# Optimization experiments

Hardware: AMD Instinct MI355X
Metric: run time of the kernel (lower is better)

Reference implementation:

```python
import jax, jax.numpy as jnp
import numpy as np

B, H, W, C = 64, 56, 56, 128
WIN, SHIFT, NH = 7, 3, 4
HD = C // NH
N = WIN * WIN
nWh, nWw = H // WIN, W // WIN
nW = nWh * nWw
MLP_H = 4 * C


def _rel_pos_index():
    # same construction as WindowAttention.__init__
    coords = np.stack(np.meshgrid(np.arange(WIN), np.arange(WIN), indexing='ij')).reshape(2, -1)
    rel = coords[:, :, None] - coords[:, None, :]
    rel = rel.transpose(1, 2, 0).copy()
    rel[..., 0] += WIN - 1
    rel[..., 1] += WIN - 1
    rel[..., 0] *= 2 * WIN - 1
    return rel.sum(-1)  # (N, N) int


def _attn_mask():
    # standard SW-MSA mask (0 / -100 like the torch reference)
    img = np.zeros((H, W))
    cnt = 0
    for hs in (slice(0, -WIN), slice(-WIN, -SHIFT), slice(-SHIFT, None)):
        for ws in (slice(0, -WIN), slice(-WIN, -SHIFT), slice(-SHIFT, None)):
            img[hs, ws] = cnt
            cnt += 1
    m = img.reshape(nWh, WIN, nWw, WIN).transpose(0, 2, 1, 3).reshape(nW, N)
    diff = m[:, None, :] - m[:, :, None]
    return np.where(diff != 0, -100.0, 0.0).astype(np.float32)  # (nW, N, N)


def _ln(x, g, b):
    mu = x.mean(-1, keepdims=True)
    var = ((x - mu) ** 2).mean(-1, keepdims=True)
    return (x - mu) / jnp.sqrt(var + 1e-5) * g + b


def setup_inputs() -> dict:
    key = jax.random.key(0)
    ks = jax.random.split(key, 6)
    s = 0.02
    return {
        'x': jax.random.normal(ks[0], (B, H * W, C), jnp.float32),
        'ln1_g': jnp.ones((C,), jnp.float32),
        'ln1_b': jnp.zeros((C,), jnp.float32),
        'qkv_w': jax.random.normal(ks[1], (3 * C, C), jnp.float32) * s,
        'qkv_b': jnp.zeros((3 * C,), jnp.float32),
        'rpb_table': jax.random.normal(ks[2], ((2 * WIN - 1) ** 2, NH), jnp.float32) * s,
        'proj_w': jax.random.normal(ks[3], (C, C), jnp.float32) * s,
        'proj_b': jnp.zeros((C,), jnp.float32),
        'ln2_g': jnp.ones((C,), jnp.float32),
        'ln2_b': jnp.zeros((C,), jnp.float32),
        'fc1_w': jax.random.normal(ks[4], (MLP_H, C), jnp.float32) * s,
        'fc1_b': jnp.zeros((MLP_H,), jnp.float32),
        'fc2_w': jax.random.normal(ks[5], (C, MLP_H), jnp.float32) * s,
        'fc2_b': jnp.zeros((C,), jnp.float32),
    }


def reference(x, ln1_g, ln1_b, qkv_w, qkv_b, rpb_table, proj_w, proj_b,
              ln2_g, ln2_b, fc1_w, fc1_b, fc2_w, fc2_b):
    rpi = jnp.asarray(_rel_pos_index())          # (N, N)
    mask = jnp.asarray(_attn_mask())             # (nW, N, N)

    shortcut = x
    h = _ln(x, ln1_g, ln1_b).reshape(B, H, W, C)
    # cyclic shift
    h = jnp.roll(h, (-SHIFT, -SHIFT), axis=(1, 2))
    # window partition -> (B*nW, N, C)
    wins = h.reshape(B, nWh, WIN, nWw, WIN, C).transpose(0, 1, 3, 2, 4, 5).reshape(B * nW, N, C)

    # window attention
    qkv = (wins @ qkv_w.T + qkv_b).reshape(B * nW, N, 3, NH, HD).transpose(2, 0, 3, 1, 4)
    q, k, v = qkv[0] * (HD ** -0.5), qkv[1], qkv[2]   # (B*nW, NH, N, HD)
    attn = jnp.einsum('bhnd,bhmd->bhnm', q, k)
    bias = rpb_table[rpi.reshape(-1)].reshape(N, N, NH).transpose(2, 0, 1)  # (NH, N, N)
    attn = attn + bias[None]
    attn = attn.reshape(B, nW, NH, N, N) + mask[None, :, None]
    attn = jax.nn.softmax(attn.reshape(B * nW, NH, N, N), axis=-1)
    o = jnp.einsum('bhnm,bhmd->bhnd', attn, v).transpose(0, 2, 1, 3).reshape(B * nW, N, C)
    o = o @ proj_w.T + proj_b

    # window reverse + reverse shift
    o = o.reshape(B, nWh, nWw, WIN, WIN, C).transpose(0, 1, 3, 2, 4, 5).reshape(B, H, W, C)
    o = jnp.roll(o, (SHIFT, SHIFT), axis=(1, 2)).reshape(B, H * W, C)

    x = shortcut + o
    # MLP residual (exact GELU, as nn.GELU default)
    h2 = _ln(x, ln2_g, ln2_b)
    h2 = jax.nn.gelu(h2 @ fc1_w.T + fc1_b, approximate=False) @ fc2_w.T + fc2_b
    return x + h2
```

## Files before the change

### kernel.cpp

```cpp
#include <hip/hip_runtime.h>
#include <math.h>

#define B_  64
#define Cc  128
#define L_  3136

typedef __bf16 b8v __attribute__((ext_vector_type(8)));
typedef __bf16 b4v __attribute__((ext_vector_type(4)));
typedef float  f4v __attribute__((ext_vector_type(4)));

__device__ __forceinline__ f4v mfma16(b8v a, b8v b, f4v c) {
    return __builtin_amdgcn_mfma_f32_16x16x32_bf16(a, b, c, 0, 0, 0);
}
__device__ __forceinline__ int region(int h, int w) {
    int a = (h < 49) ? 0 : ((h < 53) ? 1 : 2);
    int b = (w < 49) ? 0 : ((w < 53) ? 1 : 2);
    return a * 3 + b;
}

__global__ __launch_bounds__(256) void prep_kernel(
    const float* __restrict__ qkv_w, const float* __restrict__ proj_w,
    const float* __restrict__ fc1_w, const float* __restrict__ fc2_w,
    const float* __restrict__ rpb,
    __bf16* __restrict__ wsb, float* __restrict__ bm)
{
    int i = blockIdx.x * 256 + threadIdx.x;
    if      (i <  49152) wsb[i] = (__bf16)qkv_w[i];
    else if (i <  65536) wsb[i] = (__bf16)proj_w[i - 49152];
    else if (i < 131072) wsb[i] = (__bf16)fc1_w[i - 65536];
    else if (i < 196608) wsb[i] = (__bf16)fc2_w[i - 131072];
    else {
        int idx = i - 196608;
        int jj = idx & 63, ii = (idx >> 6) & 63, h = (idx >> 12) & 3, wt = idx >> 14;
        float v;
        if (jj >= 49)      v = -1e30f;
        else if (ii >= 49) v = 0.f;
        else {
            int ih = ii / 7, iw = ii - ih * 7, jh = jj / 7, jw = jj - jh * 7;
            v = rpb[((ih - jh + 6) * 13 + (iw - jw + 6)) * 4 + h];
            int WH = (wt & 2) ? 49 : 0, WW = (wt & 1) ? 49 : 0;
            if (region(WH + ih, WW + iw) != region(WH + jh, WW + jw)) v -= 100.f;
        }
        bm[idx] = v;
    }
}

__global__ __launch_bounds__(256, 3) void swin_kernel(
    const float* __restrict__ x,
    const float* __restrict__ g1, const float* __restrict__ b1,
    const float* __restrict__ qkv_b, const float* __restrict__ proj_b,
    const __bf16* __restrict__ wqkv, const __bf16* __restrict__ wproj,
    const float* __restrict__ bm,
    float* __restrict__ out)
{
    __shared__ __bf16 a_s[64 * 136];
    __shared__ __bf16 K_s[64 * 136];
    __shared__ __bf16 VT_s[128 * 72];

    const int tid = threadIdx.x, w = tid >> 6, lane = tid & 63;
    const int quad = lane >> 4, r16 = lane & 15;
    const int blk = blockIdx.x, b = blk >> 6, wi = blk & 63;
    const int wh = wi >> 3, ww = wi & 7;
    const int wt = ((wh == 7) ? 2 : 0) | ((ww == 7) ? 1 : 0);
    const float scale = 0.17677669529663687f;

    {
        f4v gg0 = *(const f4v*)(g1 + r16 * 8), gg1 = *(const f4v*)(g1 + r16 * 8 + 4);
        f4v bb0 = *(const f4v*)(b1 + r16 * 8), bb1 = *(const f4v*)(b1 + r16 * 8 + 4);
        #pragma unroll
        for (int it = 0; it < 4; it++) {
            int local = it * 4 + quad;
            int t = w * 16 + local;
            b8v o;
            #pragma unroll
            for (int e = 0; e < 8; e++) o[e] = (__bf16)0.f;
            if (t < 49) {
                int th = t / 7, tw = t - th * 7;
                int sh = wh * 7 + th + 3; if (sh >= 56) sh -= 56;
                int sw = ww * 7 + tw + 3; if (sw >= 56) sw -= 56;
                const float* xp = x + (b * L_ + sh * 56 + sw) * Cc + r16 * 8;
                f4v x0 = *(const f4v*)(xp), x1 = *(const f4v*)(xp + 4);
                float s = 0.f, q = 0.f;
                #pragma unroll
                for (int e = 0; e < 4; e++) {
                    s += x0[e] + x1[e];
                    q += x0[e] * x0[e] + x1[e] * x1[e];
                }
                s += __shfl_xor(s, 1, 64); q += __shfl_xor(q, 1, 64);
                s += __shfl_xor(s, 2, 64); q += __shfl_xor(q, 2, 64);
                s += __shfl_xor(s, 4, 64); q += __shfl_xor(q, 4, 64);
                s += __shfl_xor(s, 8, 64); q += __shfl_xor(q, 8, 64);
                float mu = s * (1.f / 128.f);
                float rs = rsqrtf(q * (1.f / 128.f) - mu * mu + 1e-5f);
                #pragma unroll
                for (int e = 0; e < 4; e++) {
                    o[e]     = (__bf16)((x0[e] - mu) * rs * gg0[e] + bb0[e]);
                    o[4 + e] = (__bf16)((x1[e] - mu) * rs * gg1[e] + bb1[e]);
                }
            }
            *(b8v*)(a_s + (w * 16 + local) * 136 + r16 * 8) = o;
        }
    }
    __syncthreads();

    b8v A[4][4];
    #pragma unroll
    for (int mt = 0; mt < 4; mt++)
        #pragma unroll
        for (int i = 0; i < 4; i++)
            A[mt][i] = *(const b8v*)(a_s + (mt * 16 + r16) * 136 + i * 32 + quad * 8);
    __syncthreads();

    #pragma unroll
    for (int nt6 = 0; nt6 < 6; nt6++) {
        const int col = w * 96 + nt6 * 16;
        const __bf16* bp = wqkv + (col + r16) * 128 + quad * 8;
        b8v B0 = *(const b8v*)(bp),      B1 = *(const b8v*)(bp + 32);
        b8v B2 = *(const b8v*)(bp + 64), B3 = *(const b8v*)(bp + 96);
        if (col < 256) {
            f4v qb = *(const f4v*)(qkv_b + col + quad * 4);
            #pragma unroll
            for (int mt = 0; mt < 4; mt++) {
                f4v acc = {0.f, 0.f, 0.f, 0.f};
                acc = mfma16(B0, A[mt][0], acc);
                acc = mfma16(B1, A[mt][1], acc);
                acc = mfma16(B2, A[mt][2], acc);
                acc = mfma16(B3, A[mt][3], acc);
                b4v pk;
                if (col < 128) {
                    #pragma unroll
                    for (int r = 0; r < 4; r++) pk[r] = (__bf16)((acc[r] + qb[r]) * scale);
                    *(b4v*)(a_s + (mt * 16 + r16) * 136 + col + quad * 4) = pk;
                } else {
                    #pragma unroll
                    for (int r = 0; r < 4; r++) pk[r] = (__bf16)(acc[r] + qb[r]);
                    *(b4v*)(K_s + (mt * 16 + r16) * 136 + (col - 128) + quad * 4) = pk;
                }
            }
        } else {
            float vb = qkv_b[col + r16];
            #pragma unroll
            for (int mt = 0; mt < 4; mt++) {
                f4v acc = {0.f, 0.f, 0.f, 0.f};
                acc = mfma16(A[mt][0], B0, acc);
                acc = mfma16(A[mt][1], B1, acc);
                acc = mfma16(A[mt][2], B2, acc);
                acc = mfma16(A[mt][3], B3, acc);
                b4v pk;
                #pragma unroll
                for (int r = 0; r < 4; r++) pk[r] = (__bf16)(acc[r] + vb);
                *(b4v*)(VT_s + (col - 256 + r16) * 72 + mt * 16 + quad * 4) = pk;
            }
        }
    }
    __syncthreads();

    b8v qf[4];
    #pragma unroll
    for (int h = 0; h < 4; h++)
        qf[h] = *(const b8v*)(a_s + (w * 16 + r16) * 136 + h * 32 + quad * 8);

    __bf16* scr = a_s + (w * 16) * 136;
    const float* bmq = bm + wt * 4 * 4096 + (w * 16 + r16) * 64;

    f4v o_acc[4][2];
    #pragma unroll
    for (int h = 0; h < 4; h++)
        #pragma unroll
        for (int n = 0; n < 2; n++)
            o_acc[h][n] = (f4v){0.f, 0.f, 0.f, 0.f};

    #pragma unroll
    for (int h = 0; h < 4; h++) {
        f4v s[4];
        #pragma unroll
        for (int nt = 0; nt < 4; nt++) {
            b8v kf = *(const b8v*)(K_s + (nt * 16 + r16) * 136 + h * 32 + quad * 8);
            f4v z = {0.f, 0.f, 0.f, 0.f};
            s[nt] = mfma16(kf, qf[h], z);
        }
        float sm = 0.f;
        #pragma unroll
        for (int nt = 0; nt < 4; nt++) {
            f4v mb = *(const f4v*)(bmq + h * 4096 + nt * 16 + quad * 4);
            #pragma unroll
            for (int r = 0; r < 4; r++) {
                s[nt][r] = __expf(s[nt][r] + mb[r]);
                sm += s[nt][r];
            }
        }
        sm += __shfl_xor(sm, 16, 64);
        sm += __shfl_xor(sm, 32, 64);
        float inv = 1.f / sm;
        #pragma unroll
        for (int nt = 0; nt < 4; nt++) {
            b4v pk;
            #pragma unroll
            for (int r = 0; r < 4; r++) pk[r] = (__bf16)(s[nt][r] * inv);
            *(b4v*)(scr + r16 * 136 + nt * 16 + quad * 4) = pk;
        }
        #pragma unroll
        for (int ks = 0; ks < 2; ks++) {
            b8v pf = *(const b8v*)(scr + r16 * 136 + ks * 32 + quad * 8);
            #pragma unroll
            for (int nt = 0; nt < 2; nt++) {
                b8v vf = *(const b8v*)(VT_s + (h * 32 + nt * 16 + r16) * 72 + ks * 32 + quad * 8);
                o_acc[h][nt] = mfma16(vf, pf, o_acc[h][nt]);
            }
        }
    }

    #pragma unroll
    for (int h = 0; h < 4; h++)
        #pragma unroll
        for (int nt = 0; nt < 2; nt++) {
            b4v pk;
            #pragma unroll
            for (int r = 0; r < 4; r++) pk[r] = (__bf16)o_acc[h][nt][r];
            *(b4v*)(scr + r16 * 136 + h * 32 + nt * 16 + quad * 4) = pk;
        }
    __syncthreads();

    {
        b8v O[4][4];
        #pragma unroll
        for (int mt = 0; mt < 4; mt++)
            #pragma unroll
            for (int i = 0; i < 4; i++)
                O[mt][i] = *(const b8v*)(a_s + (mt * 16 + r16) * 136 + i * 32 + quad * 8);

        #pragma unroll
        for (int nt = 0; nt < 2; nt++) {
            const int col = w * 32 + nt * 16;
            const __bf16* bp = wproj + (col + r16) * 128 + quad * 8;
            b8v B0 = *(const b8v*)(bp),      B1 = *(const b8v*)(bp + 32);
            b8v B2 = *(const b8v*)(bp + 64), B3 = *(const b8v*)(bp + 96);
            f4v pb = *(const f4v*)(proj_b + col + quad * 4);
            #pragma unroll
            for (int mt = 0; mt < 4; mt++) {
                f4v acc = {0.f, 0.f, 0.f, 0.f};
                acc = mfma16(B0, O[mt][0], acc);
                acc = mfma16(B1, O[mt][1], acc);
                acc = mfma16(B2, O[mt][2], acc);
                acc = mfma16(B3, O[mt][3], acc);
                int t = mt * 16 + r16;
                if (t < 49) {
                    int th = t / 7, tw = t - th * 7;
                    int sh = wh * 7 + th + 3; if (sh >= 56) sh -= 56;
                    int sw = ww * 7 + tw + 3; if (sw >= 56) sw -= 56;
                    int off = (b * L_ + sh * 56 + sw) * Cc + col + quad * 4;
                    f4v xr = *(const f4v*)(x + off);
                    f4v res;
                    #pragma unroll
                    for (int r = 0; r < 4; r++) res[r] = xr[r] + acc[r] + pb[r];
                    *(f4v*)(out + off) = res;
                }
            }
        }
    }
}

__global__ __launch_bounds__(256, 4) void mlp_kernel(
    float* __restrict__ out,
    const float* __restrict__ g2, const float* __restrict__ b2,
    const __bf16* __restrict__ wfc1, const __bf16* __restrict__ wfc2,
    const float* __restrict__ fc1_b, const float* __restrict__ fc2_b)
{
    __shared__ __bf16 x2[64 * 136];
    __shared__ __bf16 h1[64 * 136];

    const int tid = threadIdx.x, w = tid >> 6, lane = tid & 63;
    const int quad = lane >> 4, r16 = lane & 15;
    const int rowbase = blockIdx.x * 64;

    {
        const int r = tid >> 2, sub = tid & 3;
        const float* xp = out + (rowbase + r) * Cc + sub * 32;
        f4v xa[8];
        #pragma unroll
        for (int j = 0; j < 8; j++) xa[j] = *(const f4v*)(xp + j * 4);
        float s = 0.f, q = 0.f;
        #pragma unroll
        for (int j = 0; j < 8; j++)
            #pragma unroll
            for (int e = 0; e < 4; e++) { float v = xa[j][e]; s += v; q += v * v; }
        s += __shfl_xor(s, 1, 64); q += __shfl_xor(q, 1, 64);
        s += __shfl_xor(s, 2, 64); q += __shfl_xor(q, 2, 64);
        float mu = s * (1.f / 128.f);
        float rs = rsqrtf(q * (1.f / 128.f) - mu * mu + 1e-5f);
        #pragma unroll
        for (int j = 0; j < 8; j += 2) {
            int c = sub * 32 + j * 4;
            f4v gg0 = *(const f4v*)(g2 + c), gg1 = *(const f4v*)(g2 + c + 4);
            f4v bb0 = *(const f4v*)(b2 + c), bb1 = *(const f4v*)(b2 + c + 4);
            b8v o;
            #pragma unroll
            for (int e = 0; e < 4; e++) {
                o[e]     = (__bf16)((xa[j][e]     - mu) * rs * gg0[e] + bb0[e]);
                o[4 + e] = (__bf16)((xa[j + 1][e] - mu) * rs * gg1[e] + bb1[e]);
            }
            *(b8v*)(x2 + r * 136 + c) = o;
        }
    }
    __syncthreads();

    f4v acc[4][2];
    #pragma unroll
    for (int mt = 0; mt < 4; mt++)
        #pragma unroll
        for (int nt = 0; nt < 2; nt++)
            acc[mt][nt] = (f4v){0.f, 0.f, 0.f, 0.f};

    for (int hc = 0; hc < 4; hc++) {
        {
            b8v Bf[2][4]; f4v b14[2];
            #pragma unroll
            for (int nt = 0; nt < 2; nt++) {
                const int col = hc * 128 + w * 32 + nt * 16;
                const __bf16* bp = wfc1 + (col + r16) * 128 + quad * 8;
                Bf[nt][0] = *(const b8v*)(bp);      Bf[nt][1] = *(const b8v*)(bp + 32);
                Bf[nt][2] = *(const b8v*)(bp + 64); Bf[nt][3] = *(const b8v*)(bp + 96);
                b14[nt] = *(const f4v*)(fc1_b + col + quad * 4);
            }
            #pragma unroll
            for (int mt = 0; mt < 4; mt++) {
                const __bf16* ap = x2 + (mt * 16 + r16) * 136 + quad * 8;
                b8v A0 = *(const b8v*)(ap),      A1 = *(const b8v*)(ap + 32);
                b8v A2 = *(const b8v*)(ap + 64), A3 = *(const b8v*)(ap + 96);
                #pragma unroll
                for (int nt = 0; nt < 2; nt++) {
                    f4v a = {0.f, 0.f, 0.f, 0.f};
                    a = mfma16(Bf[nt][0], A0, a);
                    a = mfma16(Bf[nt][1], A1, a);
                    a = mfma16(Bf[nt][2], A2, a);
                    a = mfma16(Bf[nt][3], A3, a);
                    b4v pk;
                    #pragma unroll
                    for (int r = 0; r < 4; r++) {
                        float v = a[r] + b14[nt][r];
                        v = 0.5f * v * (1.f + erff(v * 0.70710678118654752f));
                        pk[r] = (__bf16)v;
                    }
                    *(b4v*)(h1 + (mt * 16 + r16) * 136 + w * 32 + nt * 16 + quad * 4) = pk;
                }
            }
        }
        __syncthreads();
        #pragma unroll
        for (int Ks = 0; Ks < 4; Ks++) {
            b8v Af[4];
            #pragma unroll
            for (int mt = 0; mt < 4; mt++)
                Af[mt] = *(const b8v*)(h1 + (mt * 16 + r16) * 136 + Ks * 32 + quad * 8);
            #pragma unroll
            for (int nt = 0; nt < 2; nt++) {
                const __bf16* bp = wfc2 + (w * 32 + nt * 16 + r16) * 512
                                 + hc * 128 + Ks * 32 + quad * 8;
                b8v Bf = *(const b8v*)(bp);
                #pragma unroll
                for (int mt = 0; mt < 4; mt++)
                    acc[mt][nt] = mfma16(Bf, Af[mt], acc[mt][nt]);
            }
        }
        if (hc < 3) __syncthreads();
    }

    #pragma unroll
    for (int nt = 0; nt < 2; nt++) {
        const int col = w * 32 + nt * 16 + quad * 4;
        f4v fb = *(const f4v*)(fc2_b + col);
        #pragma unroll
        for (int mt = 0; mt < 4; mt++) {
            float* op = out + (rowbase + mt * 16 + r16) * Cc + col;
            f4v v = *(const f4v*)op;
            #pragma unroll
            for (int r = 0; r < 4; r++) v[r] += acc[mt][nt][r] + fb[r];
            *(f4v*)op = v;
        }
    }
}

extern "C" void kernel_launch(void* const* d_in, const int* in_sizes, int n_in,
                              void* d_out, int out_size, void* d_ws, size_t ws_size,
                              hipStream_t stream) {
    __bf16* wsb = (__bf16*)d_ws;
    float*  bmp = (float*)((char*)d_ws + 393216);
    prep_kernel<<<1024, 256, 0, stream>>>(
        (const float*)d_in[3], (const float*)d_in[6],
        (const float*)d_in[10], (const float*)d_in[12],
        (const float*)d_in[5], wsb, bmp);
    swin_kernel<<<B_ * 64, 256, 0, stream>>>(
        (const float*)d_in[0],
        (const float*)d_in[1], (const float*)d_in[2],
        (const float*)d_in[4], (const float*)d_in[7],
        wsb, wsb + 49152,
        bmp, (float*)d_out);
    mlp_kernel<<<(B_ * L_) / 64, 256, 0, stream>>>(
        (float*)d_out,
        (const float*)d_in[8], (const float*)d_in[9],
        wsb + 65536, wsb + 131072,
        (const float*)d_in[11], (const float*)d_in[13]);
}
```

Before: 467.0 us.

## Swizzle LDS tiles, use tanh-form GELU, raise MLP occupancy

Shared-memory tiles in both kernels drop the 136-element row padding and use an XOR swizzle on the column (row&7 shifted into 8-element groups). This avoids bank conflicts and shrinks LDS use. The exact erf GELU is replaced by the tanh-approximation written as a sigmoid with __expf, which is cheaper per element but deviates slightly from exact GELU. The MLP kernel's launch bounds minimum blocks rises from 4 to 5 to allow more resident blocks, at the risk of register pressure.

```diff
diff --git a/kernel.cpp b/kernel.cpp
--- a/kernel.cpp
+++ b/kernel.cpp
@@ -16,6 +16,14 @@
     int a = (h < 49) ? 0 : ((h < 53) ? 1 : 2);
     int b = (w < 49) ? 0 : ((w < 53) ? 1 : 2);
     return a * 3 + b;
+}
+__device__ __forceinline__ int swz(int row, int col) {
+    return row * 128 + (col ^ ((row & 7) << 3));
+}
+__device__ __forceinline__ float gelu_f(float v) {
+    float s = v * v;
+    float u = v * (1.5957691216057308f + 0.07135481987f * s);
+    return v / (1.f + __expf(-u));
 }
 
 __global__ __launch_bounds__(256) void prep_kernel(
@@ -53,8 +61,8 @@
     const float* __restrict__ bm,
     float* __restrict__ out)
 {
-    __shared__ __bf16 a_s[64 * 136];
-    __shared__ __bf16 K_s[64 * 136];
+    __shared__ __bf16 a_s[64 * 128];
+    __shared__ __bf16 K_s[64 * 128];
     __shared__ __bf16 VT_s[128 * 72];
 
     const int tid = threadIdx.x, w = tid >> 6, lane = tid & 63;
@@ -98,7 +106,7 @@
                     o[4 + e] = (__bf16)((x1[e] - mu) * rs * gg1[e] + bb1[e]);
                 }
             }
-            *(b8v*)(a_s + (w * 16 + local) * 136 + r16 * 8) = o;
+            *(b8v*)(&a_s[swz(w * 16 + local, r16 * 8)]) = o;
         }
     }
     __syncthreads();
@@ -108,7 +116,7 @@
     for (int mt = 0; mt < 4; mt++)
         #pragma unroll
         for (int i = 0; i < 4; i++)
-            A[mt][i] = *(const b8v*)(a_s + (mt * 16 + r16) * 136 + i * 32 + quad * 8);
+            A[mt][i] = *(const b8v*)&a_s[swz(mt * 16 + r16, i * 32 + quad * 8)];
     __syncthreads();
 
     #pragma unroll
@@ -130,11 +138,11 @@
                 if (col < 128) {
                     #pragma unroll
                     for (int r = 0; r < 4; r++) pk[r] = (__bf16)((acc[r] + qb[r]) * scale);
-                    *(b4v*)(a_s + (mt * 16 + r16) * 136 + col + quad * 4) = pk;
+                    *(b4v*)&a_s[swz(mt * 16 + r16, col + quad * 4)] = pk;
                 } else {
                     #pragma unroll
                     for (int r = 0; r < 4; r++) pk[r] = (__bf16)(acc[r] + qb[r]);
-                    *(b4v*)(K_s + (mt * 16 + r16) * 136 + (col - 128) + quad * 4) = pk;
+                    *(b4v*)&K_s[swz(mt * 16 + r16, (col - 128) + quad * 4)] = pk;
                 }
             }
         } else {
@@ -158,9 +166,8 @@
     b8v qf[4];
     #pragma unroll
     for (int h = 0; h < 4; h++)
-        qf[h] = *(const b8v*)(a_s + (w * 16 + r16) * 136 + h * 32 + quad * 8);
-
-    __bf16* scr = a_s + (w * 16) * 136;
+        qf[h] = *(const b8v*)&a_s[swz(w * 16 + r16, h * 32 + quad * 8)];
+
     const float* bmq = bm + wt * 4 * 4096 + (w * 16 + r16) * 64;
 
     f4v o_acc[4][2];
@@ -175,7 +182,7 @@
         f4v s[4];
         #pragma unroll
         for (int nt = 0; nt < 4; nt++) {
-            b8v kf = *(const b8v*)(K_s + (nt * 16 + r16) * 136 + h * 32 + quad * 8);
+            b8v kf = *(const b8v*)&K_s[swz(nt * 16 + r16, h * 32 + quad * 8)];
             f4v z = {0.f, 0.f, 0.f, 0.f};
             s[nt] = mfma16(kf, qf[h], z);
         }
@@ -197,11 +204,11 @@
             b4v pk;
             #pragma unroll
             for (int r = 0; r < 4; r++) pk[r] = (__bf16)(s[nt][r] * inv);
-            *(b4v*)(scr + r16 * 136 + nt * 16 + quad * 4) = pk;
+            *(b4v*)&a_s[swz(w * 16 + r16, nt * 16 + quad * 4)] = pk;
         }
         #pragma unroll
         for (int ks = 0; ks < 2; ks++) {
-            b8v pf = *(const b8v*)(scr + r16 * 136 + ks * 32 + quad * 8);
+            b8v pf = *(const b8v*)&a_s[swz(w * 16 + r16, ks * 32 + quad * 8)];
             #pragma unroll
             for (int nt = 0; nt < 2; nt++) {
                 b8v vf = *(const b8v*)(VT_s + (h * 32 + nt * 16 + r16) * 72 + ks * 32 + quad * 8);
@@ -217,7 +224,7 @@
             b4v pk;
             #pragma unroll
             for (int r = 0; r < 4; r++) pk[r] = (__bf16)o_acc[h][nt][r];
-            *(b4v*)(scr + r16 * 136 + h * 32 + nt * 16 + quad * 4) = pk;
+            *(b4v*)&a_s[swz(w * 16 + r16, h * 32 + nt * 16 + quad * 4)] = pk;
         }
     __syncthreads();
 
@@ -227,7 +234,7 @@
         for (int mt = 0; mt < 4; mt++)
             #pragma unroll
             for (int i = 0; i < 4; i++)
-                O[mt][i] = *(const b8v*)(a_s + (mt * 16 + r16) * 136 + i * 32 + quad * 8);
+                O[mt][i] = *(const b8v*)&a_s[swz(mt * 16 + r16, i * 32 + quad * 8)];
 
         #pragma unroll
         for (int nt = 0; nt < 2; nt++) {
@@ -260,14 +267,14 @@
     }
 }
 
-__global__ __launch_bounds__(256, 4) void mlp_kernel(
+__global__ __launch_bounds__(256, 5) void mlp_kernel(
     float* __restrict__ out,
     const float* __restrict__ g2, const float* __restrict__ b2,
     const __bf16* __restrict__ wfc1, const __bf16* __restrict__ wfc2,
     const float* __restrict__ fc1_b, const float* __restrict__ fc2_b)
 {
-    __shared__ __bf16 x2[64 * 136];
-    __shared__ __bf16 h1[64 * 136];
+    __shared__ __bf16 x2[64 * 128];
+    __shared__ __bf16 h1[64 * 128];
 
     const int tid = threadIdx.x, w = tid >> 6, lane = tid & 63;
     const int quad = lane >> 4, r16 = lane & 15;
@@ -299,7 +306,7 @@
                 o[e]     = (__bf16)((xa[j][e]     - mu) * rs * gg0[e] + bb0[e]);
                 o[4 + e] = (__bf16)((xa[j + 1][e] - mu) * rs * gg1[e] + bb1[e]);
             }
-            *(b8v*)(x2 + r * 136 + c) = o;
+            *(b8v*)(&x2[swz(r, c)]) = o;
         }
     }
     __syncthreads();
@@ -324,9 +331,10 @@
             }
             #pragma unroll
             for (int mt = 0; mt < 4; mt++) {
-                const __bf16* ap = x2 + (mt * 16 + r16) * 136 + quad * 8;
-                b8v A0 = *(const b8v*)(ap),      A1 = *(const b8v*)(ap + 32);
-                b8v A2 = *(const b8v*)(ap + 64), A3 = *(const b8v*)(ap + 96);
+                b8v A0 = *(const b8v*)&x2[swz(mt * 16 + r16, quad * 8)];
+                b8v A1 = *(const b8v*)&x2[swz(mt * 16 + r16, quad * 8 + 32)];
+                b8v A2 = *(const b8v*)&x2[swz(mt * 16 + r16, quad * 8 + 64)];
+                b8v A3 = *(const b8v*)&x2[swz(mt * 16 + r16, quad * 8 + 96)];
                 #pragma unroll
                 for (int nt = 0; nt < 2; nt++) {
                     f4v a = {0.f, 0.f, 0.f, 0.f};
@@ -336,12 +344,9 @@
                     a = mfma16(Bf[nt][3], A3, a);
                     b4v pk;
                     #pragma unroll
-                    for (int r = 0; r < 4; r++) {
-                        float v = a[r] + b14[nt][r];
-                        v = 0.5f * v * (1.f + erff(v * 0.70710678118654752f));
-                        pk[r] = (__bf16)v;
-                    }
-                    *(b4v*)(h1 + (mt * 16 + r16) * 136 + w * 32 + nt * 16 + quad * 4) = pk;
+                    for (int r = 0; r < 4; r++)
+                        pk[r] = (__bf16)gelu_f(a[r] + b14[nt][r]);
+                    *(b4v*)&h1[swz(mt * 16 + r16, w * 32 + nt * 16 + quad * 4)] = pk;
                 }
             }
         }
@@ -351,7 +356,7 @@
             b8v Af[4];
             #pragma unroll
             for (int mt = 0; mt < 4; mt++)
-                Af[mt] = *(const b8v*)(h1 + (mt * 16 + r16) * 136 + Ks * 32 + quad * 8);
+                Af[mt] = *(const b8v*)&h1[swz(mt * 16 + r16, Ks * 32 + quad * 8)];
             #pragma unroll
             for (int nt = 0; nt < 2; nt++) {
                 const __bf16* bp = wfc2 + (w * 32 + nt * 16 + r16) * 512
```

Result: slower. 523.0 us (+12.0%).
